# Performance work log

Hardware: AMD Instinct MI355X
Metric: run time of the kernel (lower is better)

The kernel has to match this reference:

```python
import jax, jax.numpy as jnp
import numpy as np

LATENT_SIZE = 1024
WORD_SIZE = 64
NB_WORD = 8192
COMMIT_VQ = 2.5
BATCH = 2048


def setup_inputs() -> dict:
    key = jax.random.key(0)
    k1, k2, k3 = jax.random.split(key, 3)
    z_mean = jax.random.normal(k1, (BATCH, LATENT_SIZE), dtype=jnp.float32)
    z_log_var = jax.random.normal(k2, (BATCH, LATENT_SIZE), dtype=jnp.float32)
    # Embedding initialized uniform(-1/nb_word, 1/nb_word) in the torch module;
    # use normal here for a numerically non-degenerate correctness baseline.
    emb_weight = jax.random.normal(k3, (NB_WORD, WORD_SIZE), dtype=jnp.float32)
    return {"z_mean": z_mean, "z_log_var": z_log_var, "emb_weight": emb_weight}


def reference(z_mean, z_log_var, emb_weight):
    sg = jax.lax.stop_gradient
    input_shape = z_mean.shape
    # (B * latent/word, word)
    z = z_mean.reshape(-1, LATENT_SIZE // WORD_SIZE, WORD_SIZE)
    z_flat = z.reshape(-1, WORD_SIZE)
    # squared euclidean distances: (N, nb_word)
    distances = (
        jnp.sum(z_flat ** 2, axis=1, keepdims=True)
        + jnp.sum(emb_weight ** 2, axis=1)
        - 2.0 * jnp.einsum("bd,nd->bn", z_flat, emb_weight)
    )
    min_idx = jnp.argmin(distances, axis=1)  # (N,)
    z_q = emb_weight[min_idx].reshape(z.shape)  # gather codebook vectors
    loss = (
        jnp.mean((sg(z_q) - z) ** 2)
        + COMMIT_VQ * jnp.mean((z_q - sg(z)) ** 2)
    )
    z_q_st = z + sg(z_q - z)  # straight-through estimator
    return z_q_st.reshape(input_shape), loss
```

## Files before the change

kernel.cpp:

```cpp
#include <hip/hip_runtime.h>
#include <math.h>

#define LATENT   1024
#define WORD     64
#define NB_WORD  8192
#define BATCH    2048
#define NROWS    (BATCH * LATENT / WORD)
#define NELEM    (BATCH * LATENT)

#define NCHUNK   8
#define CWCHUNK  (NB_WORD / NCHUNK)
#define TPC      (CWCHUNK / 16)
#define NTILE    (NB_WORD / 16)
#define PKTS     (NTILE * 6 * 64)

typedef __attribute__((ext_vector_type(8))) __bf16 bf16x8;
typedef __attribute__((ext_vector_type(4))) float  f32x4;

__global__ __launch_bounds__(256) void vq_e2_kernel(
    const float* __restrict__ emb, float* __restrict__ e2) {
    int m = blockIdx.x * 256 + threadIdx.x;
    if (m >= NB_WORD) return;
    const float4* ep = reinterpret_cast<const float4*>(emb + (size_t)m * WORD);
    float s0 = 0.f, s1 = 0.f, s2 = 0.f, s3 = 0.f;
#pragma unroll
    for (int i = 0; i < 16; ++i) {
        float4 v = ep[i];
        s0 = fmaf(v.x, v.x, s0);
        s1 = fmaf(v.y, v.y, s1);
        s2 = fmaf(v.z, v.z, s2);
        s3 = fmaf(v.w, v.w, s3);
    }
    e2[m] = (s0 + s1) + (s2 + s3);
}

__global__ __launch_bounds__(256) void vq_epack_kernel(
    const float* __restrict__ emb, bf16x8* __restrict__ epack) {
    int p = blockIdx.x * 256 + threadIdx.x;
    int lane = p & 63;
    int q    = p >> 6;
    int Ks   = q & 1;
    int r    = q >> 1;
    int spl  = r % 3;
    int tile = r / 3;
    int cw = tile * 16 + (lane & 15);
    int k0 = Ks * 32 + (lane >> 4) * 8;
    const float4* s4 = reinterpret_cast<const float4*>(emb + (size_t)cw * WORD + k0);
    float4 a = s4[0], b = s4[1];
    float tv[8] = {a.x, a.y, a.z, a.w, b.x, b.y, b.z, b.w};
    bf16x8 o;
#pragma unroll
    for (int e = 0; e < 8; ++e) {
        float v = tv[e];
        __bf16 h  = (__bf16)v;
        float r1  = v - (float)h;
        __bf16 m  = (__bf16)r1;
        float r2  = r1 - (float)m;
        __bf16 lo = (__bf16)r2;
        o[e] = (spl == 0) ? h : ((spl == 1) ? m : lo);
    }
    epack[p] = o;
}

__device__ __forceinline__ void gload_lds16(const char* g, char* l) {
    __builtin_amdgcn_global_load_lds(
        (const __attribute__((address_space(1))) void*)g,
        (__attribute__((address_space(3))) void*)l, 16, 0, 0);
}

__global__ __launch_bounds__(256)
__attribute__((amdgpu_waves_per_eu(4, 8)))
void vq_argmin_kernel(
    const float* __restrict__ z, const bf16x8* __restrict__ epack,
    const float* __restrict__ e2, unsigned long long* __restrict__ best) {

    __shared__ __align__(16) char le[2 * 6144];
    __shared__ __align__(16) float le2c[CWCHUNK];

    const int tid   = threadIdx.x;
    const int lane  = tid & 63;
    const int wband = tid >> 6;
    const int l15   = lane & 15;
    const int l4    = lane >> 4;
    const int rowbase   = blockIdx.x * 128 + wband * 32;
    const int tile0     = blockIdx.y * TPC;
    const int chunkbase = blockIdx.y * CWCHUNK;

    {
        const char* src = (const char*)epack + (size_t)tile0 * 6144 + tid * 16;
        char* dst = le + (tid & ~63) * 16;
        gload_lds16(src, dst);
        if (tid < 128) gload_lds16(src + 4096, dst + 4096);
    }
    gload_lds16((const char*)(e2 + chunkbase + tid * 4),
                (char*)le2c + (tid & ~63) * 16);

    bf16x8 A[2][2][3];
    const float4* zf4 = reinterpret_cast<const float4*>(z);
#pragma unroll
    for (int mt = 0; mt < 2; ++mt) {
        int row = rowbase + mt * 16 + l15;
#pragma unroll
        for (int Ks = 0; Ks < 2; ++Ks) {
            float4 v0 = zf4[(size_t)row * 16 + Ks * 8 + l4 * 2];
            float4 v1 = zf4[(size_t)row * 16 + Ks * 8 + l4 * 2 + 1];
            float tv[8] = {v0.x, v0.y, v0.z, v0.w, v1.x, v1.y, v1.z, v1.w};
#pragma unroll
            for (int e = 0; e < 8; ++e) {
                float v = tv[e];
                __bf16 h  = (__bf16)v;
                float r1  = v - (float)h;
                __bf16 m  = (__bf16)r1;
                float r2  = r1 - (float)m;
                __bf16 lo = (__bf16)r2;
                A[mt][Ks][0][e] = h;
                A[mt][Ks][1][e] = m;
                A[mt][Ks][2][e] = lo;
            }
        }
    }
    __syncthreads();

    float bestd[8] = {INFINITY, INFINITY, INFINITY, INFINITY,
                      INFINITY, INFINITY, INFINITY, INFINITY};
    int   bt[8]    = {0, 0, 0, 0, 0, 0, 0, 0};

    for (int t = 0; t < TPC; ++t) {
        const int buf = t & 1;
        if (t + 1 < TPC) {
            const char* src = (const char*)epack +
                              (size_t)(tile0 + t + 1) * 6144 + tid * 16;
            char* dst = le + (buf ^ 1) * 6144 + (tid & ~63) * 16;
            gload_lds16(src, dst);
            if (tid < 128) gload_lds16(src + 4096, dst + 4096);
        }
        float e2v = le2c[t * 16 + l15];

        f32x4 acc0 = {0.f, 0.f, 0.f, 0.f};
        f32x4 acc1 = {0.f, 0.f, 0.f, 0.f};
#pragma unroll
        for (int Ks = 0; Ks < 2; ++Ks) {
            const char* bbase = le + buf * 6144 + (size_t)Ks * 1024 + lane * 16;
            bf16x8 Bh = *reinterpret_cast<const bf16x8*>(bbase);
            bf16x8 Bm = *reinterpret_cast<const bf16x8*>(bbase + 2048);
            bf16x8 Bl = *reinterpret_cast<const bf16x8*>(bbase + 4096);
            acc0 = __builtin_amdgcn_mfma_f32_16x16x32_bf16(A[0][Ks][0], Bh, acc0, 0, 0, 0);
            acc1 = __builtin_amdgcn_mfma_f32_16x16x32_bf16(A[1][Ks][0], Bh, acc1, 0, 0, 0);
            acc0 = __builtin_amdgcn_mfma_f32_16x16x32_bf16(A[0][Ks][1], Bh, acc0, 0, 0, 0);
            acc1 = __builtin_amdgcn_mfma_f32_16x16x32_bf16(A[1][Ks][1], Bh, acc1, 0, 0, 0);
            acc0 = __builtin_amdgcn_mfma_f32_16x16x32_bf16(A[0][Ks][2], Bh, acc0, 0, 0, 0);
            acc1 = __builtin_amdgcn_mfma_f32_16x16x32_bf16(A[1][Ks][2], Bh, acc1, 0, 0, 0);
            acc0 = __builtin_amdgcn_mfma_f32_16x16x32_bf16(A[0][Ks][0], Bm, acc0, 0, 0, 0);
            acc1 = __builtin_amdgcn_mfma_f32_16x16x32_bf16(A[1][Ks][0], Bm, acc1, 0, 0, 0);
            acc0 = __builtin_amdgcn_mfma_f32_16x16x32_bf16(A[0][Ks][1], Bm, acc0, 0, 0, 0);
            acc1 = __builtin_amdgcn_mfma_f32_16x16x32_bf16(A[1][Ks][1], Bm, acc1, 0, 0, 0);
            acc0 = __builtin_amdgcn_mfma_f32_16x16x32_bf16(A[0][Ks][0], Bl, acc0, 0, 0, 0);
            acc1 = __builtin_amdgcn_mfma_f32_16x16x32_bf16(A[1][Ks][0], Bl, acc1, 0, 0, 0);
        }

#pragma unroll
        for (int v = 0; v < 4; ++v) {
            float d0 = fmaf(-2.0f, acc0[v], e2v);
            if (d0 < bestd[v])     { bestd[v]     = d0; bt[v]     = t; }
            float d1 = fmaf(-2.0f, acc1[v], e2v);
            if (d1 < bestd[4 + v]) { bestd[4 + v] = d1; bt[4 + v] = t; }
        }
        __syncthreads();
    }

#pragma unroll
    for (int mt = 0; mt < 2; ++mt) {
#pragma unroll
        for (int v = 0; v < 4; ++v) {
            float bd = bestd[mt * 4 + v];
            int   cw = chunkbase + bt[mt * 4 + v] * 16 + l15;
            unsigned db = __float_as_uint(bd);
            db = (db & 0x80000000u) ? ~db : (db | 0x80000000u);
            unsigned long long key =
                ((unsigned long long)db << 32) | (unsigned)cw;
#pragma unroll
            for (int off = 1; off < 16; off <<= 1) {
                unsigned long long o = __shfl_xor(key, off);
                key = (o < key) ? o : key;
            }
            if (l15 == 0)
                atomicMin(&best[rowbase + mt * 16 + l4 * 4 + v], key);
        }
    }
}

__global__ __launch_bounds__(256) void vq_out_kernel(
    const float* __restrict__ z, const float* __restrict__ emb,
    const unsigned long long* __restrict__ best,
    float* __restrict__ out, float* __restrict__ lsum) {
    const int base = (blockIdx.x * 256 + threadIdx.x) * 8;
    const int row  = base >> 6;
    const int m    = (int)(best[row] & 0xFFFFFFFFull);

    const float4* zp = reinterpret_cast<const float4*>(z + base);
    const float4* qp = reinterpret_cast<const float4*>(emb + (size_t)m * WORD + (base & 63));
    float4* op = reinterpret_cast<float4*>(out + base);

    float s = 0.f;
#pragma unroll
    for (int i = 0; i < 2; ++i) {
        float4 zv = zp[i];
        float4 qv = qp[i];
        float dx = qv.x - zv.x, dy = qv.y - zv.y, dz = qv.z - zv.z, dw = qv.w - zv.w;
        float4 ov;
        ov.x = zv.x + dx; ov.y = zv.y + dy; ov.z = zv.z + dz; ov.w = zv.w + dw;
        op[i] = ov;
        s += dx*dx + dy*dy + dz*dz + dw*dw;
    }

#pragma unroll
    for (int off = 32; off > 0; off >>= 1) s += __shfl_down(s, off);
    __shared__ float wsum[4];
    int lane = threadIdx.x & 63, wid = threadIdx.x >> 6;
    if (lane == 0) wsum[wid] = s;
    __syncthreads();
    if (threadIdx.x == 0)
        atomicAdd(lsum, (wsum[0] + wsum[1]) + (wsum[2] + wsum[3]));
}

__global__ void vq_loss_kernel(const float* __restrict__ lsum,
                               float* __restrict__ loss_out) {
    float mean = lsum[0] * (1.0f / (float)NELEM);
    loss_out[0] = mean + 2.5f * mean;
}

extern "C" void kernel_launch(void* const* d_in, const int* in_sizes, int n_in,
                              void* d_out, int out_size, void* d_ws, size_t ws_size,
                              hipStream_t stream) {
    const float* z   = (const float*)d_in[0];
    const float* emb = (const float*)d_in[2];
    float* out = (float*)d_out;

    bf16x8* epack = (bf16x8*)d_ws;
    float*  e2    = (float*)((char*)d_ws + (size_t)PKTS * 16);
    unsigned long long* best =
        (unsigned long long*)((char*)e2 + NB_WORD * sizeof(float));
    float* lsum = (float*)((char*)best + NROWS * sizeof(unsigned long long));

    hipMemsetAsync(best, 0xFF, NROWS * sizeof(unsigned long long), stream);
    hipMemsetAsync(lsum, 0, sizeof(float), stream);

    vq_e2_kernel<<<NB_WORD / 256, 256, 0, stream>>>(emb, e2);
    vq_epack_kernel<<<PKTS / 256, 256, 0, stream>>>(emb, epack);
    vq_argmin_kernel<<<dim3(NROWS / 128, NCHUNK), 256, 0, stream>>>(
        z, epack, e2, best);
    vq_out_kernel<<<NELEM / (256 * 8), 256, 0, stream>>>(z, emb, best, out, lsum);
    vq_loss_kernel<<<1, 1, 0, stream>>>(lsum, out + NELEM);
}
```

Baseline: 195.1 us.

## Restructure codebook LDS double-buffer pipeline with explicit waitcnt and single barrier

Moves the first codebook tile load after the A-fragment conversion and replaces the per-iteration trailing __syncthreads with an explicit vmcnt(0) wait plus s_barrier placed before issuing the next tile's global-to-LDS load. The e2 values are read directly from global memory instead of being staged in LDS. It also raises wave priority around the MFMA block. The aim is fewer barriers and more overlap of loads with compute, at the cost of an extra redundant load on the last iteration and per-iteration global reads of e2.

Result: slower. 208.7 us (+7.0%).

```diff
diff --git a/kernel.cpp b/kernel.cpp
--- a/kernel.cpp
+++ b/kernel.cpp
@@ -75,7 +75,6 @@
     const float* __restrict__ e2, unsigned long long* __restrict__ best) {
 
     __shared__ __align__(16) char le[2 * 6144];
-    __shared__ __align__(16) float le2c[CWCHUNK];
 
     const int tid   = threadIdx.x;
     const int lane  = tid & 63;
@@ -85,15 +84,7 @@
     const int rowbase   = blockIdx.x * 128 + wband * 32;
     const int tile0     = blockIdx.y * TPC;
     const int chunkbase = blockIdx.y * CWCHUNK;
-
-    {
-        const char* src = (const char*)epack + (size_t)tile0 * 6144 + tid * 16;
-        char* dst = le + (tid & ~63) * 16;
-        gload_lds16(src, dst);
-        if (tid < 128) gload_lds16(src + 4096, dst + 4096);
-    }
-    gload_lds16((const char*)(e2 + chunkbase + tid * 4),
-                (char*)le2c + (tid & ~63) * 16);
+    const float* e2g    = e2 + chunkbase;
 
     bf16x8 A[2][2][3];
     const float4* zf4 = reinterpret_cast<const float4*>(z);
@@ -119,7 +110,14 @@
             }
         }
     }
-    __syncthreads();
+
+    {
+        const char* src = (const char*)epack + (size_t)tile0 * 6144;
+        gload_lds16(src + wband * 1024 + lane * 16, le + wband * 1024);
+        if (wband < 2)
+            gload_lds16(src + (4 + wband) * 1024 + lane * 16,
+                        le + (4 + wband) * 1024);
+    }
 
     float bestd[8] = {INFINITY, INFINITY, INFINITY, INFINITY,
                       INFINITY, INFINITY, INFINITY, INFINITY};
@@ -127,17 +125,25 @@
 
     for (int t = 0; t < TPC; ++t) {
         const int buf = t & 1;
-        if (t + 1 < TPC) {
-            const char* src = (const char*)epack +
-                              (size_t)(tile0 + t + 1) * 6144 + tid * 16;
-            char* dst = le + (buf ^ 1) * 6144 + (tid & ~63) * 16;
-            gload_lds16(src, dst);
-            if (tid < 128) gload_lds16(src + 4096, dst + 4096);
-        }
-        float e2v = le2c[t * 16 + l15];
+        float e2v = e2g[t * 16 + l15];
+
+        asm volatile("s_waitcnt vmcnt(0)" ::: "memory");
+        __builtin_amdgcn_sched_barrier(0);
+        __builtin_amdgcn_s_barrier();
+
+        {
+            const int tn = (t + 1 < TPC) ? (t + 1) : t;
+            const char* src = (const char*)epack + (size_t)(tile0 + tn) * 6144;
+            char* dst = le + (buf ^ 1) * 6144;
+            gload_lds16(src + wband * 1024 + lane * 16, dst + wband * 1024);
+            if (wband < 2)
+                gload_lds16(src + (4 + wband) * 1024 + lane * 16,
+                            dst + (4 + wband) * 1024);
+        }
 
         f32x4 acc0 = {0.f, 0.f, 0.f, 0.f};
         f32x4 acc1 = {0.f, 0.f, 0.f, 0.f};
+        __builtin_amdgcn_s_setprio(1);
 #pragma unroll
         for (int Ks = 0; Ks < 2; ++Ks) {
             const char* bbase = le + buf * 6144 + (size_t)Ks * 1024 + lane * 16;
@@ -157,6 +163,7 @@
             acc0 = __builtin_amdgcn_mfma_f32_16x16x32_bf16(A[0][Ks][0], Bl, acc0, 0, 0, 0);
             acc1 = __builtin_amdgcn_mfma_f32_16x16x32_bf16(A[1][Ks][0], Bl, acc1, 0, 0, 0);
         }
+        __builtin_amdgcn_s_setprio(0);
 
 #pragma unroll
         for (int v = 0; v < 4; ++v) {
@@ -165,7 +172,6 @@
             float d1 = fmaf(-2.0f, acc1[v], e2v);
             if (d1 < bestd[4 + v]) { bestd[4 + v] = d1; bt[4 + v] = t; }
         }
-        __syncthreads();
     }
 
 #pragma unroll
```
